# Performance work log

Hardware: AMD Instinct MI355X
Metric: run time of the kernel (lower is better)

## Reference

```python
import jax, jax.numpy as jnp
import numpy as np

B, C, H, W = 32, 256, 7, 7
HEADS = 8
DIM_HEAD = 64
INNER = HEADS * DIM_HEAD  # 512
N_ANGLES = 16
KS = 5
GROUPS = 32
EPS = 1e-5


def setup_inputs() -> dict:
    key = jax.random.key(0)
    ks = jax.random.split(key, 16)
    w = lambda k, shp: jax.random.normal(k, shp, jnp.float32) * 0.05
    return {
        'x': jax.random.normal(ks[0], (B, C, H, W), jnp.float32),
        'gn_g': jnp.ones((C,), jnp.float32), 'gn_b': jnp.zeros((C,), jnp.float32),
        'sa_w1': w(ks[1], (C // 8, C)), 'sa_b1': jnp.zeros((C // 8,), jnp.float32),
        'sa_w2': w(ks[2], (C, C // 8)), 'sa_b2': jnp.zeros((C,), jnp.float32),
        'sa_gn_g': jnp.ones((C,), jnp.float32), 'sa_gn_b': jnp.zeros((C,), jnp.float32),
        'ra_gn_g': jnp.ones((C,), jnp.float32), 'ra_gn_b': jnp.zeros((C,), jnp.float32),
        'ra_qkv_w': w(ks[3], (3 * C, C)),
        'ra_proj_w': w(ks[4], (C, C)), 'ra_proj_b': jnp.zeros((C,), jnp.float32),
        'aa_ln_g': jnp.ones((C,), jnp.float32), 'aa_ln_b': jnp.zeros((C,), jnp.float32),
        'aa_qkv_w': w(ks[5], (3 * INNER, C)),
        'aa_relpos': w(ks[6], (2 * 7 - 1, 2 * 7 - 1, HEADS)),
        'aa_out_w': w(ks[7], (C, INNER)), 'aa_out_b': jnp.zeros((C,), jnp.float32),
        'ad_dir_w': w(ks[8], (N_ANGLES, C, C, KS, KS)),
        'ad_ap_w1': w(ks[9], (128, C)), 'ad_ap_b1': jnp.zeros((128,), jnp.float32),
        'ad_ap_w2': w(ks[10], (N_ANGLES, 128)), 'ad_ap_b2': jnp.zeros((N_ANGLES,), jnp.float32),
        'ad_proj_w': w(ks[11], (C, C)), 'ad_proj_b': jnp.zeros((C,), jnp.float32),
        'gate_w': w(ks[12], (4, C)), 'gate_b': jnp.zeros((4,), jnp.float32),
        'proj_w': w(ks[13], (C, C)), 'proj_b': jnp.zeros((C,), jnp.float32),
    }


def _gn(x, g, b):
    Bx, Cx, Hx, Wx = x.shape
    xr = x.reshape(Bx, GROUPS, -1)
    m = xr.mean(-1, keepdims=True)
    v = xr.var(-1, keepdims=True)
    xn = ((xr - m) * jax.lax.rsqrt(v + EPS)).reshape(Bx, Cx, Hx, Wx)
    return xn * g[None, :, None, None] + b[None, :, None, None]


def _c1(x, w, b=None):
    y = jnp.einsum('bchw,oc->bohw', x, w)
    return y if b is None else y + b[None, :, None, None]


def _rot_attn_pass(x, qkv_w):
    Bx, Cx, Hx, Wx = x.shape
    d = Cx // HEADS
    q, k, v = jnp.split(_c1(x, qkv_w), 3, axis=1)
    sh = lambda t: t.reshape(Bx, HEADS, d, Hx * Wx).transpose(0, 1, 3, 2)  # b h n d
    q, k, v = sh(q), sh(k), sh(v)
    a = jax.nn.softmax(jnp.einsum('bhid,bhjd->bhij', q, k) * (d ** -0.5), axis=-1)
    o = jnp.einsum('bhij,bhjd->bhid', a, v)
    return o.transpose(0, 1, 3, 2).reshape(Bx, Cx, Hx, Wx)


def _forward(x, gn_g, gn_b, sa_w1, sa_b1, sa_w2, sa_b2, sa_gn_g, sa_gn_b,
             ra_gn_g, ra_gn_b, ra_qkv_w, ra_proj_w, ra_proj_b,
             aa_ln_g, aa_ln_b, aa_qkv_w, aa_relpos, aa_out_w, aa_out_b,
             ad_dir_w, ad_ap_w1, ad_ap_b1, ad_ap_w2, ad_ap_b2, ad_proj_w, ad_proj_b,
             gate_w, gate_b, proj_w, proj_b):
    normed = _gn(x, gn_g, gn_b)

    # --- SpatialAttention branch ---
    wts = jax.nn.sigmoid(_c1(jax.nn.relu(_c1(normed, sa_w1, sa_b1)), sa_w2, sa_b2))
    spatial = _gn(normed * wts + normed, sa_gn_g, sa_gn_b)

    # --- RotationAwareAttention branch: 4 rot90 passes, max-fused ---
    xr = _gn(normed, ra_gn_g, ra_gn_b)
    r0 = _rot_attn_pass(xr, ra_qkv_w)
    r1 = jnp.rot90(_rot_attn_pass(jnp.rot90(xr, 1, (2, 3)), ra_qkv_w), 3, (2, 3))
    r2 = jnp.rot90(_rot_attn_pass(jnp.rot90(xr, 2, (2, 3)), ra_qkv_w), 2, (2, 3))
    r3 = jnp.rot90(_rot_attn_pass(jnp.rot90(xr, 3, (2, 3)), ra_qkv_w), 1, (2, 3))
    mx = jnp.maximum(jnp.maximum(r0, r1), jnp.maximum(r2, r3))
    rotation = _c1(mx, ra_proj_w, ra_proj_b) + normed

    # --- AngleAwareSelfAttention branch (rel-pos-biased MHSA over 49 tokens) ---
    Nn = H * W
    t = normed.reshape(B, C, Nn).transpose(0, 2, 1)  # [B,N,C]
    mu = t.mean(-1, keepdims=True)
    var = t.var(-1, keepdims=True)
    tn = (t - mu) * jax.lax.rsqrt(var + EPS) * aa_ln_g + aa_ln_b
    q, k, v = jnp.split(jnp.einsum('bnc,oc->bno', tn, aa_qkv_w), 3, axis=-1)
    sh = lambda u: u.reshape(B, Nn, HEADS, DIM_HEAD).transpose(0, 2, 1, 3)
    q, k, v = sh(q), sh(k), sh(v)
    dots = jnp.einsum('bhid,bhjd->bhij', q, k) * (DIM_HEAD ** -0.5)
    idx = jnp.arange(Nn)
    yi, xi = idx // W, idx % W
    dy = yi[None, :] - yi[:, None] + (H - 1)  # offsets into 13x13 table
    dx = xi[None, :] - xi[:, None] + (W - 1)
    bias = aa_relpos[dy, dx].transpose(2, 0, 1)[None]  # [1,heads,N,N]
    attn = jax.nn.softmax(dots + bias, axis=-1)
    o = jnp.einsum('bhij,bhjd->bhid', attn, v).transpose(0, 2, 1, 3).reshape(B, Nn, INNER)
    o = jnp.einsum('bni,oi->bno', o, aa_out_w) + aa_out_b
    angle = o.transpose(0, 2, 1).reshape(B, C, H, W) + normed

    # --- AngleAdaptiveAttention branch: 16 directional 5x5 convs + learned softmax gate ---
    dir_out = jax.lax.conv_general_dilated(
        normed, ad_dir_w.reshape(N_ANGLES * C, C, KS, KS), (1, 1), 'SAME',
        dimension_numbers=('NCHW', 'OIHW', 'NCHW')).reshape(B, N_ANGLES, C, H, W)
    gap = normed.mean((2, 3))  # [B,C]
    h1 = jax.nn.relu(gap @ ad_ap_w1.T + ad_ap_b1)
    aw = jax.nn.softmax(h1 @ ad_ap_w2.T + ad_ap_b2, axis=1)  # [B,16]
    comb = jnp.einsum('bkchw,bk->bchw', dir_out, aw)
    adaptive = _c1(comb, ad_proj_w, ad_proj_b) + normed

    # --- gated fusion ---
    gates = jax.nn.softmax(_c1(x, gate_w, gate_b), axis=1)  # [B,4,H,W]
    fused = (spatial * gates[:, 0:1] + rotation * gates[:, 1:2]
             + angle * gates[:, 2:3] + adaptive * gates[:, 3:4])
    return _c1(fused, proj_w, proj_b) + x


def reference(x, gn_g, gn_b, sa_w1, sa_b1, sa_w2, sa_b2, sa_gn_g, sa_gn_b,
              ra_gn_g, ra_gn_b, ra_qkv_w, ra_proj_w, ra_proj_b,
              aa_ln_g, aa_ln_b, aa_qkv_w, aa_relpos, aa_out_w, aa_out_b,
              ad_dir_w, ad_ap_w1, ad_ap_b1, ad_ap_w2, ad_ap_b2, ad_proj_w, ad_proj_b,
              gate_w, gate_b, proj_w, proj_b):
    return _forward(x, gn_g, gn_b, sa_w1, sa_b1, sa_w2, sa_b2, sa_gn_g, sa_gn_b,
                    ra_gn_g, ra_gn_b, ra_qkv_w, ra_proj_w, ra_proj_b,
                    aa_ln_g, aa_ln_b, aa_qkv_w, aa_relpos, aa_out_w, aa_out_b,
                    ad_dir_w, ad_ap_w1, ad_ap_b1, ad_ap_w2, ad_ap_b2, ad_proj_w, ad_proj_b,
                    gate_w, gate_b, proj_w, proj_b)
```

## Files before the change

kernel.cpp:

```cpp
#include <hip/hip_runtime.h>

#define EPS 1e-5f
typedef unsigned short u16;
typedef unsigned int u32;
typedef float f32x4 __attribute__((ext_vector_type(4)));
typedef short bf16x8 __attribute__((ext_vector_type(8)));
typedef unsigned int u32x2 __attribute__((ext_vector_type(2)));

__device__ __forceinline__ float bf2f(u16 h){
  return __uint_as_float(((u32)h) << 16);
}
__device__ __forceinline__ u16 f2bf(float f){
  u32 u = __float_as_uint(f);
  u += 0x7fffu + ((u >> 16) & 1u);
  return (u16)(u >> 16);
}
__device__ __forceinline__ u32 pk2(float lo, float hi){
  return ((u32)f2bf(hi) << 16) | (u32)f2bf(lo);
}
union BF8 { bf16x8 v; u32 u[4]; };

__global__ __launch_bounds__(256) void k_prep1(
    const float* __restrict__ x, const float* __restrict__ gn_g, const float* __restrict__ gn_b,
    const float* __restrict__ ra_g, const float* __restrict__ ra_b,
    float* __restrict__ normed, float* __restrict__ xr, float* __restrict__ gap)
{
  int ch = blockIdx.x, b = blockIdx.y;
  int c0 = ch * 32;
  __shared__ float xs[1568], ns[1568];
  const float* xb = x + ((size_t)b * 256 + c0) * 49;
  for (int i = threadIdx.x; i < 1568; i += 256) xs[i] = xb[i];
  __syncthreads();
  int wv = threadIdx.x >> 6, lane = threadIdx.x & 63;
  const float* gsrc = xs + wv * 392;
  float* ndst = ns + wv * 392;
  float s = 0.f, ss = 0.f;
  for (int i = lane; i < 392; i += 64){ float v = gsrc[i]; s += v; ss += v * v; }
  for (int off = 32; off; off >>= 1){ s += __shfl_down(s, off); ss += __shfl_down(ss, off); }
  s = __shfl(s, 0); ss = __shfl(ss, 0);
  float m = s / 392.f, rs = rsqrtf(ss / 392.f - m * m + EPS);
  for (int i = lane; i < 392; i += 64){
    int c = c0 + wv * 8 + i / 49;
    ndst[i] = (gsrc[i] - m) * rs * gn_g[c] + gn_b[c];
  }
  __syncthreads();
  float* nb = normed + ((size_t)b * 256 + c0) * 49;
  for (int i = threadIdx.x; i < 1568; i += 256) nb[i] = ns[i];
  if (threadIdx.x < 32){
    float g2 = 0.f; const float* rp = ns + threadIdx.x * 49;
    for (int p = 0; p < 49; p++) g2 += rp[p];
    gap[(size_t)b * 256 + c0 + threadIdx.x] = g2 * (1.f / 49.f);
  }
  s = 0.f; ss = 0.f;
  for (int i = lane; i < 392; i += 64){ float v = ndst[i]; s += v; ss += v * v; }
  for (int off = 32; off; off >>= 1){ s += __shfl_down(s, off); ss += __shfl_down(ss, off); }
  s = __shfl(s, 0); ss = __shfl(ss, 0);
  m = s / 392.f; rs = rsqrtf(ss / 392.f - m * m + EPS);
  float* xrb = xr + ((size_t)b * 256 + c0) * 49;
  for (int i = lane; i < 392; i += 64){
    int c = c0 + wv * 8 + i / 49;
    xrb[wv * 392 + i] = (ndst[i] - m) * rs * ra_g[c] + ra_b[c];
  }
}

__device__ void dev_pos(
    const float* __restrict__ x, const float* __restrict__ normed,
    const float* __restrict__ gate_w, const float* __restrict__ gate_b,
    float* __restrict__ gates_g, float* __restrict__ lnm_g, float* __restrict__ lnr_g,
    int pc, int b, float* sm)
{
  float* gw = sm;
  for (int i = threadIdx.x; i < 1024; i += 256) gw[i] = gate_w[i];
  __syncthreads();
  int wv = threadIdx.x >> 6, lane = threadIdx.x & 63;
  for (int pi = wv; pi < 7; pi += 4){
    int p = pc * 7 + pi;
    const float* nb = normed + (size_t)b * 12544 + p;
    const float* xb = x + (size_t)b * 12544 + p;
    float s = 0.f, ss = 0.f, g0 = 0.f, g1 = 0.f, g2 = 0.f, g3 = 0.f;
    for (int c = lane; c < 256; c += 64){
      float nv = nb[c * 49];
      float xv = xb[c * 49];
      s += nv; ss += nv * nv;
      g0 += xv * gw[c]; g1 += xv * gw[256 + c];
      g2 += xv * gw[512 + c]; g3 += xv * gw[768 + c];
    }
    for (int off = 32; off; off >>= 1){
      s += __shfl_down(s, off); ss += __shfl_down(ss, off);
      g0 += __shfl_down(g0, off); g1 += __shfl_down(g1, off);
      g2 += __shfl_down(g2, off); g3 += __shfl_down(g3, off);
    }
    if (lane == 0){
      float mu = s / 256.f;
      lnm_g[b * 49 + p] = mu;
      lnr_g[b * 49 + p] = rsqrtf(ss / 256.f - mu * mu + EPS);
      g0 += gate_b[0]; g1 += gate_b[1]; g2 += gate_b[2]; g3 += gate_b[3];
      float mx = fmaxf(fmaxf(g0, g1), fmaxf(g2, g3));
      float e0 = __expf(g0 - mx), e1 = __expf(g1 - mx), e2 = __expf(g2 - mx), e3 = __expf(g3 - mx);
      float inv = 1.f / (e0 + e1 + e2 + e3);
      float* gg = gates_g + (size_t)b * 196 + p;
      gg[0] = e0 * inv; gg[49] = e1 * inv; gg[98] = e2 * inv; gg[147] = e3 * inv;
    }
  }
}

__device__ void dev_h1aw(
    const float* __restrict__ normed, const float* __restrict__ sa_w1, const float* __restrict__ sa_b1,
    const float* __restrict__ ap_w1, const float* __restrict__ ap_b1,
    const float* __restrict__ ap_w2, const float* __restrict__ ap_b2,
    const float* __restrict__ gap_g,
    float* __restrict__ h1_g, float* __restrict__ aw_g,
    int xb2, int b, float* sm)
{
  int t = threadIdx.x;
  if (xb2 == 7){
    float* gaps = sm; float* h = sm + 256; float* lg = sm + 384;
    gaps[t] = gap_g[b * 256 + t];
    __syncthreads();
    if (t < 128){
      float s = ap_b1[t];
      const float* wr = ap_w1 + t * 256;
      #pragma unroll 4
      for (int c = 0; c < 256; c++) s += gaps[c] * wr[c];
      h[t] = fmaxf(s, 0.f);
    }
    __syncthreads();
    if (t < 16){
      float s = ap_b2[t];
      const float* wr = ap_w2 + t * 128;
      #pragma unroll 4
      for (int o = 0; o < 128; o++) s += h[o] * wr[o];
      lg[t] = s;
    }
    __syncthreads();
    if (t == 0){
      float mx = -1e30f;
      for (int k = 0; k < 16; k++) mx = fmaxf(mx, lg[k]);
      float e[16], smm = 0.f;
      for (int k = 0; k < 16; k++){ e[k] = __expf(lg[k] - mx); smm += e[k]; }
      float inv = 1.f / smm;
      for (int k = 0; k < 16; k++) aw_g[b * 16 + k] = e[k] * inv;
    }
    return;
  }
  float* w1t = sm;
  float* ns2 = sm + 8448;
  int p0 = xb2 * 7;
  for (int i = t; i < 8192; i += 256){
    int o = i >> 8, c = i & 255;
    w1t[c * 33 + o] = sa_w1[i];
  }
  for (int i = t; i < 1792; i += 256){
    int c = i / 7, pl = i - c * 7;
    ns2[i] = normed[(size_t)b * 12544 + c * 49 + p0 + pl];
  }
  __syncthreads();
  if (t < 224){
    int pl = t >> 5, o = t & 31;
    float s = sa_b1[o];
    #pragma unroll 8
    for (int c = 0; c < 256; c++) s += ns2[c * 7 + pl] * w1t[c * 33 + o];
    h1_g[(size_t)b * 1568 + (p0 + pl) * 32 + o] = fmaxf(s, 0.f);
  }
}

__global__ __launch_bounds__(256) void k_pre2(
    const float* __restrict__ x, const float* __restrict__ normed,
    const float* __restrict__ gate_w, const float* __restrict__ gate_b,
    const float* __restrict__ sa_w1, const float* __restrict__ sa_b1,
    const float* __restrict__ ap_w1, const float* __restrict__ ap_b1,
    const float* __restrict__ ap_w2, const float* __restrict__ ap_b2,
    const float* __restrict__ gap_g,
    float* __restrict__ gates_g, float* __restrict__ lnm_g, float* __restrict__ lnr_g,
    float* __restrict__ h1_g, float* __restrict__ aw_g)
{
  __shared__ float sm[10240];
  int bx = blockIdx.x, b = blockIdx.y;
  if (bx < 7)
    dev_pos(x, normed, gate_w, gate_b, gates_g, lnm_g, lnr_g, bx, b, sm);
  else
    dev_h1aw(normed, sa_w1, sa_b1, ap_w1, ap_b1, ap_w2, ap_b2, gap_g, h1_g, aw_g, bx - 7, b, sm);
}

__device__ void dev_spatial(
    const float* __restrict__ normed, const float* __restrict__ h1_g,
    const float* __restrict__ sa_w2, const float* __restrict__ sa_b2,
    const float* __restrict__ sa_g, const float* __restrict__ sa_bb,
    float* __restrict__ spat_g, int gc, int b, float* sm)
{
  float* h1s = sm;
  float* w2s = sm + 1617;
  int t = threadIdx.x;
  for (int i = t; i < 1568; i += 256){
    int p = i >> 5, o = i & 31;
    h1s[p * 33 + o] = h1_g[(size_t)b * 1568 + i];
  }
  for (int i = t; i < 1024; i += 256) w2s[i] = sa_w2[gc * 1024 + i];
  __syncthreads();
  int wv = t >> 6, lane = t & 63;
  int cg0 = wv * 8;
  const float* nb = normed + (size_t)b * 12544 + (gc * 32 + cg0) * 49;
  float tmp[7];
  float s = 0.f, ss = 0.f;
  #pragma unroll
  for (int j = 0; j < 7; j++){
    int i = lane + 64 * j;
    float v = 0.f;
    if (i < 392){
      int c = i / 49;
      const float* wr = w2s + (cg0 + c) * 32;
      const float* hp = h1s + (i - c * 49) * 33;
      float d = sa_b2[gc * 32 + cg0 + c];
      #pragma unroll
      for (int o = 0; o < 32; o++) d += hp[o] * wr[o];
      v = nb[i] * (1.f + 1.f / (1.f + __expf(-d)));
      s += v; ss += v * v;
    }
    tmp[j] = v;
  }
  for (int off = 32; off; off >>= 1){ s += __shfl_down(s, off); ss += __shfl_down(ss, off); }
  s = __shfl(s, 0); ss = __shfl(ss, 0);
  float m = s / 392.f, rs = rsqrtf(ss / 392.f - m * m + EPS);
  float* sb = spat_g + (size_t)b * 12544 + (gc * 32 + cg0) * 49;
  #pragma unroll
  for (int j = 0; j < 7; j++){
    int i = lane + 64 * j;
    if (i < 392){
      int c = gc * 32 + cg0 + i / 49;
      sb[i] = (tmp[j] - m) * rs * sa_g[c] + sa_bb[c];
    }
  }
}

__device__ void dev_weff(
    const float* __restrict__ W, const float* __restrict__ aw, u16* __restrict__ weff, int bx)
{
  const size_t t = ((size_t)bx * 256 + threadIdx.x) * 4;
  float4 A[16];
  #pragma unroll
  for (int k = 0; k < 16; k++) A[k] = *(const float4*)(W + (size_t)k * 1638400 + t);
  #pragma unroll 1
  for (int b = 0; b < 32; b++){
    float s0 = 0.f, s1 = 0.f, s2 = 0.f, s3 = 0.f;
    #pragma unroll
    for (int k = 0; k < 16; k++){
      float a = aw[b * 16 + k];
      s0 += a * A[k].x; s1 += a * A[k].y; s2 += a * A[k].z; s3 += a * A[k].w;
    }
    u32x2 o; o.x = pk2(s0, s1); o.y = pk2(s2, s3);
    __builtin_nontemporal_store(o, (u32x2*)(weff + (size_t)b * 1638400 + t));
  }
}

__device__ void dev_im2col(
    const float* __restrict__ normed, u16* __restrict__ xim, int p, int b, float* sm)
{
  u16* row = (u16*)sm;
  int ci = threadIdx.x;
  int py = p / 7, px = p - py * 7;
  const float* nb = normed + (size_t)b * 12544 + ci * 49;
  u16* rp = row + ci * 25;
  #pragma unroll
  for (int sy = 0; sy < 5; sy++){
    int iy = py + sy - 2;
    #pragma unroll
    for (int sx = 0; sx < 5; sx++){
      int ix = px + sx - 2;
      float v = (iy >= 0 && iy < 7 && ix >= 0 && ix < 7) ? nb[iy * 7 + ix] : 0.f;
      rp[sy * 5 + sx] = f2bf(v);
    }
  }
  __syncthreads();
  const u32* rs = (const u32*)row;
  u32* od = (u32*)(xim + (size_t)(b * 49 + p) * 6400);
  for (int i = threadIdx.x; i < 3200; i += 256) od[i] = rs[i];
}

__device__ __forceinline__ void mfma_gemm_dev(
    const float* __restrict__ W, const float* __restrict__ bias,
    const float* __restrict__ act, const float* __restrict__ res,
    float* __restrict__ out, int M, int K, int m0blk, int p0, int b,
    const float* __restrict__ lnm, const float* __restrict__ lnr,
    const float* __restrict__ lng, const float* __restrict__ lnb)
{
  int wv = threadIdx.x >> 6, lane = threadIdx.x & 63;
  int lo = lane & 15, hi = lane >> 4;
  int m0 = m0blk + wv * 32;
  int p = p0 + lo;
  bool pok = p < 49;
  const float* ab = act + (size_t)b * K * 49;
  float lm = 0.f, lr = 0.f;
  if (lng && pok){ lm = lnm[p]; lr = lnr[p]; }
  f32x4 acc0 = {0.f, 0.f, 0.f, 0.f};
  f32x4 acc1 = {0.f, 0.f, 0.f, 0.f};
  const float* wr0 = W + (size_t)(m0 + lo) * K + hi * 8;
  const float* wr1 = W + (size_t)(m0 + 16 + lo) * K + hi * 8;
  for (int k0 = 0; k0 < K; k0 += 32){
    int kb = k0 + hi * 8;
    float4 a0lo = *(const float4*)(wr0 + k0);
    float4 a0hi = *(const float4*)(wr0 + k0 + 4);
    float4 a1lo = *(const float4*)(wr1 + k0);
    float4 a1hi = *(const float4*)(wr1 + k0 + 4);
    float bv[8];
    if (pok){
      const float* ap = ab + (size_t)kb * 49 + p;
      #pragma unroll
      for (int i = 0; i < 8; i++) bv[i] = ap[i * 49];
      if (lng){
        #pragma unroll
        for (int i = 0; i < 8; i++) bv[i] = (bv[i] - lm) * lr * lng[kb + i] + lnb[kb + i];
      }
    } else {
      #pragma unroll
      for (int i = 0; i < 8; i++) bv[i] = 0.f;
    }
    BF8 A0, A1, B;
    A0.u[0] = pk2(a0lo.x, a0lo.y); A0.u[1] = pk2(a0lo.z, a0lo.w);
    A0.u[2] = pk2(a0hi.x, a0hi.y); A0.u[3] = pk2(a0hi.z, a0hi.w);
    A1.u[0] = pk2(a1lo.x, a1lo.y); A1.u[1] = pk2(a1lo.z, a1lo.w);
    A1.u[2] = pk2(a1hi.x, a1hi.y); A1.u[3] = pk2(a1hi.z, a1hi.w);
    B.u[0] = pk2(bv[0], bv[1]); B.u[1] = pk2(bv[2], bv[3]);
    B.u[2] = pk2(bv[4], bv[5]); B.u[3] = pk2(bv[6], bv[7]);
    acc0 = __builtin_amdgcn_mfma_f32_16x16x32_bf16(A0.v, B.v, acc0, 0, 0, 0);
    acc1 = __builtin_amdgcn_mfma_f32_16x16x32_bf16(A1.v, B.v, acc1, 0, 0, 0);
  }
  if (pok){
    #pragma unroll
    for (int r = 0; r < 4; r++){
      int m = m0 + hi * 4 + r;
      size_t idx = ((size_t)b * M + m) * 49 + p;
      float v = acc0[r] + (bias ? bias[m] : 0.f);
      if (res) v += res[idx];
      out[idx] = v;
      int m2 = m + 16;
      size_t idx2 = idx + 16 * 49;
      float v2 = acc1[r] + (bias ? bias[m2] : 0.f);
      if (res) v2 += res[idx2];
      out[idx2] = v2;
    }
  }
}

__global__ __launch_bounds__(256) void k_mega1(
    const float* __restrict__ ad_dir_w, const float* __restrict__ aw, u16* __restrict__ weff,
    const float* __restrict__ ra_w, const float* __restrict__ aa_w,
    const float* __restrict__ xr, const float* __restrict__ normed,
    const float* __restrict__ lnm, const float* __restrict__ lnr,
    const float* __restrict__ ln_g, const float* __restrict__ ln_b,
    float* __restrict__ ra_qkv, float* __restrict__ aa_qkv,
    u16* __restrict__ xim,
    const float* __restrict__ h1_g, const float* __restrict__ sa_w2, const float* __restrict__ sa_b2,
    const float* __restrict__ sa_g, const float* __restrict__ sa_bb, float* __restrict__ spat_g)
{
  __shared__ float sm[3300];
  int id = blockIdx.x;
  if (id < 1600){
    dev_weff(ad_dir_w, aw, weff, id);
  } else if (id < 3904){
    int q = id - 1600;
    int bx = q % 72, b = q / 72;
    if (bx < 24){
      int m0 = (bx >> 2) * 128, p0 = (bx & 3) * 16;
      mfma_gemm_dev(ra_w, nullptr, xr, nullptr, ra_qkv, 768, 256, m0, p0, b,
                    nullptr, nullptr, nullptr, nullptr);
    } else {
      int bx2 = bx - 24;
      int m0 = (bx2 >> 2) * 128, p0 = (bx2 & 3) * 16;
      mfma_gemm_dev(aa_w, nullptr, normed, nullptr, aa_qkv, 1536, 256, m0, p0, b,
                    lnm + b * 49, lnr + b * 49, ln_g, ln_b);
    }
  } else if (id < 5472){
    int q = id - 3904;
    dev_im2col(normed, xim, q % 49, q / 49, sm);
  } else {
    int q = id - 5472;
    dev_spatial(normed, h1_g, sa_w2, sa_b2, sa_g, sa_bb, spat_g, q % 8, q / 8, sm);
  }
}

__device__ void dev_conv(
    const u16* __restrict__ weff, const u16* __restrict__ xim, float* __restrict__ partial,
    int bx, int b)
{
  int mblk = bx >> 3, kp = bx & 7;
  int wv = threadIdx.x >> 6, lane = threadIdx.x & 63;
  int lo = lane & 15, hi = lane >> 4;
  int co0 = mblk * 128 + wv * 32;
  const u16* wr0 = weff + (size_t)b * 1638400 + (size_t)(co0 + lo) * 6400 + kp * 800 + hi * 8;
  const u16* wr1 = wr0 + 16 * 6400;
  const u16* xb = xim + (size_t)b * 313600 + (size_t)lo * 6400 + kp * 800 + hi * 8;
  f32x4 acc[2][4];
  #pragma unroll
  for (int mi = 0; mi < 2; mi++)
    #pragma unroll
    for (int pi = 0; pi < 4; pi++) acc[mi][pi] = (f32x4){0.f, 0.f, 0.f, 0.f};
  #pragma unroll 1
  for (int ks = 0; ks < 25; ks++){
    int k0 = ks * 32;
    bf16x8 A0 = __builtin_nontemporal_load((const bf16x8*)(wr0 + k0));
    bf16x8 A1 = __builtin_nontemporal_load((const bf16x8*)(wr1 + k0));
    bf16x8 B0 = *(const bf16x8*)(xb + k0);
    bf16x8 B1 = *(const bf16x8*)(xb + 16 * 6400 + k0);
    bf16x8 B2 = *(const bf16x8*)(xb + 32 * 6400 + k0);
    bf16x8 B3 = *(const bf16x8*)(xb + 48 * 6400 + k0);
    acc[0][0] = __builtin_amdgcn_mfma_f32_16x16x32_bf16(A0, B0, acc[0][0], 0, 0, 0);
    acc[0][1] = __builtin_amdgcn_mfma_f32_16x16x32_bf16(A0, B1, acc[0][1], 0, 0, 0);
    acc[0][2] = __builtin_amdgcn_mfma_f32_16x16x32_bf16(A0, B2, acc[0][2], 0, 0, 0);
    acc[0][3] = __builtin_amdgcn_mfma_f32_16x16x32_bf16(A0, B3, acc[0][3], 0, 0, 0);
    acc[1][0] = __builtin_amdgcn_mfma_f32_16x16x32_bf16(A1, B0, acc[1][0], 0, 0, 0);
    acc[1][1] = __builtin_amdgcn_mfma_f32_16x16x32_bf16(A1, B1, acc[1][1], 0, 0, 0);
    acc[1][2] = __builtin_amdgcn_mfma_f32_16x16x32_bf16(A1, B2, acc[1][2], 0, 0, 0);
    acc[1][3] = __builtin_amdgcn_mfma_f32_16x16x32_bf16(A1, B3, acc[1][3], 0, 0, 0);
  }
  float* pb = partial + ((size_t)kp * 32 + b) * 12544;
  #pragma unroll
  for (int mi = 0; mi < 2; mi++){
    #pragma unroll
    for (int pi = 0; pi < 4; pi++){
      int p = pi * 16 + lo;
      if (p < 49){
        #pragma unroll
        for (int r = 0; r < 4; r++){
          int co = co0 + mi * 16 + hi * 4 + r;
          pb[co * 49 + p] = acc[mi][pi][r];
        }
      }
    }
  }
}

__device__ __forceinline__ void softmax_rows(float* sc, int tid)
{
  int r = tid >> 2, q = tid & 3;
  if (r < 49){
    float* row = sc + r * 52;
    float mx = -1e30f;
    for (int j = q; j < 49; j += 4) mx = fmaxf(mx, row[j]);
    mx = fmaxf(mx, __shfl_xor(mx, 1));
    mx = fmaxf(mx, __shfl_xor(mx, 2));
    float sm = 0.f;
    for (int j = q; j < 49; j += 4){ float e = __expf(row[j] - mx); row[j] = e; sm += e; }
    sm += __shfl_xor(sm, 1);
    sm += __shfl_xor(sm, 2);
    float inv = 1.f / sm;
    for (int j = q; j < 49; j += 4) row[j] *= inv;
  }
}

__device__ void dev_attn(
    const float* __restrict__ ra_qkv, const float* __restrict__ aa_qkv,
    const float* __restrict__ relpos,
    float* __restrict__ r0, float* __restrict__ ao,
    int xb2, int b, float* sm)
{
  if (xb2 < 8){
    int hd = xb2;
    float* qs = sm; float* ks = sm + 1617; float* vs = sm + 3234; float* sc = sm + 4851;
    const float* base = ra_qkv + (size_t)b * 768 * 49;
    for (int i = threadIdx.x; i < 1568; i += 256){
      int d = i / 49, tok = i - d * 49;
      qs[tok * 33 + d] = base[(hd * 32 + d) * 49 + tok];
      ks[tok * 33 + d] = base[(256 + hd * 32 + d) * 49 + tok];
      vs[tok * 33 + d] = base[(512 + hd * 32 + d) * 49 + tok];
    }
    __syncthreads();
    const float scale = 0.17677669529663687f;
    for (int it = threadIdx.x; it < 2401; it += 256){
      int i = it / 49, j = it - i * 49;
      float s = 0.f;
      #pragma unroll
      for (int d = 0; d < 32; d++) s += qs[i * 33 + d] * ks[j * 33 + d];
      sc[i * 52 + j] = s * scale;
    }
    __syncthreads();
    softmax_rows(sc, threadIdx.x);
    __syncthreads();
    for (int it = threadIdx.x; it < 1568; it += 256){
      int d = it / 49, i = it - d * 49;
      float o = 0.f;
      for (int j = 0; j < 49; j++) o += sc[i * 52 + j] * vs[j * 33 + d];
      r0[((size_t)b * 256 + hd * 32 + d) * 49 + i] = o;
    }
  } else {
    int hd = xb2 - 8;
    float* qs = sm; float* ks = sm + 3185; float* vs = sm + 6370; float* sc = sm + 9555;
    const float* base = aa_qkv + (size_t)b * 1536 * 49;
    for (int i = threadIdx.x; i < 3136; i += 256){
      int d = i / 49, tok = i - d * 49;
      qs[tok * 65 + d] = base[(hd * 64 + d) * 49 + tok];
      ks[tok * 65 + d] = base[(512 + hd * 64 + d) * 49 + tok];
      vs[tok * 65 + d] = base[(1024 + hd * 64 + d) * 49 + tok];
    }
    __syncthreads();
    for (int it = threadIdx.x; it < 2401; it += 256){
      int i = it / 49, j = it - i * 49;
      float s = 0.f;
      #pragma unroll
      for (int d = 0; d < 64; d++) s += qs[i * 65 + d] * ks[j * 65 + d];
      int dy = j / 7 - i / 7 + 6, dx = j % 7 - i % 7 + 6;
      sc[i * 52 + j] = s * 0.125f + relpos[(dy * 13 + dx) * 8 + hd];
    }
    __syncthreads();
    softmax_rows(sc, threadIdx.x);
    __syncthreads();
    for (int it = threadIdx.x; it < 3136; it += 256){
      int d = it / 49, i = it - d * 49;
      float o = 0.f;
      for (int j = 0; j < 49; j++) o += sc[i * 52 + j] * vs[j * 65 + d];
      ao[((size_t)b * 512 + hd * 64 + d) * 49 + i] = o;
    }
  }
}

__global__ __launch_bounds__(256) void k_mega2(
    const u16* __restrict__ weff, const u16* __restrict__ xim, float* __restrict__ partial,
    const float* __restrict__ ra_qkv, const float* __restrict__ aa_qkv,
    const float* __restrict__ relpos, float* __restrict__ r0, float* __restrict__ ao)
{
  __shared__ float sm[12103];
  int id = blockIdx.x;
  if (id < 512){
    dev_conv(weff, xim, partial, id % 16, id / 16);
  } else {
    int q = id - 512;
    dev_attn(ra_qkv, aa_qkv, relpos, r0, ao, q % 16, q / 16, sm);
  }
}

__global__ __launch_bounds__(256) void k_conv_reduce(
    const float* __restrict__ part, float* __restrict__ comb)
{
  int i = blockIdx.x * 256 + threadIdx.x;
  if (i >= 100352) return;
  float a0 = 0.f, a1 = 0.f, a2 = 0.f, a3 = 0.f;
  #pragma unroll
  for (int p = 0; p < 8; p++){
    float4 v = ((const float4*)part)[(size_t)p * 100352 + i];
    a0 += v.x; a1 += v.y; a2 += v.z; a3 += v.w;
  }
  float4 o; o.x = a0; o.y = a1; o.z = a2; o.w = a3;
  ((float4*)comb)[i] = o;
}

__global__ __launch_bounds__(256) void k_proj3(
    const float* __restrict__ ra_pw, const float* __restrict__ ra_pb, const float* __restrict__ r0,
    const float* __restrict__ aa_ow, const float* __restrict__ aa_ob, const float* __restrict__ aa_o,
    const float* __restrict__ ad_pw, const float* __restrict__ ad_pb, const float* __restrict__ comb,
    const float* __restrict__ normed,
    float* __restrict__ rotf, float* __restrict__ angf, float* __restrict__ adpf)
{
  int bx = blockIdx.x, b = blockIdx.y;
  if (bx < 8){
    int m0 = (bx >> 2) * 128, p0 = (bx & 3) * 16;
    mfma_gemm_dev(ra_pw, ra_pb, r0, normed, rotf, 256, 256, m0, p0, b,
                  nullptr, nullptr, nullptr, nullptr);
  } else if (bx < 16){
    int bx2 = bx - 8;
    int m0 = (bx2 >> 2) * 128, p0 = (bx2 & 3) * 16;
    mfma_gemm_dev(aa_ow, aa_ob, aa_o, normed, angf, 256, 512, m0, p0, b,
                  nullptr, nullptr, nullptr, nullptr);
  } else {
    int bx2 = bx - 16;
    int m0 = (bx2 >> 2) * 128, p0 = (bx2 & 3) * 16;
    mfma_gemm_dev(ad_pw, ad_pb, comb, normed, adpf, 256, 256, m0, p0, b,
                  nullptr, nullptr, nullptr, nullptr);
  }
}

__global__ __launch_bounds__(256) void k_final(
    const float* __restrict__ proj_w, const float* __restrict__ proj_b,
    const float* __restrict__ spat, const float* __restrict__ rotf,
    const float* __restrict__ angf, const float* __restrict__ adpf,
    const float* __restrict__ gates, const float* __restrict__ x,
    float* __restrict__ out)
{
  int bx = blockIdx.x, b = blockIdx.y;
  int wv = threadIdx.x >> 6, lane = threadIdx.x & 63;
  int lo = lane & 15, hi = lane >> 4;
  int m0 = (bx >> 2) * 128 + wv * 32;
  int p0 = (bx & 3) * 16;
  int p = p0 + lo;
  bool pok = p < 49;
  float g0 = 0.f, g1 = 0.f, g2 = 0.f, g3 = 0.f;
  if (pok){
    const float* g = gates + (size_t)b * 196 + p;
    g0 = g[0]; g1 = g[49]; g2 = g[98]; g3 = g[147];
  }
  size_t boff = (size_t)b * 12544;
  f32x4 acc0 = {0.f, 0.f, 0.f, 0.f};
  f32x4 acc1 = {0.f, 0.f, 0.f, 0.f};
  const float* wr0 = proj_w + (size_t)(m0 + lo) * 256 + hi * 8;
  const float* wr1 = wr0 + 16 * 256;
  for (int k0 = 0; k0 < 256; k0 += 32){
    int kb = k0 + hi * 8;
    float4 a0lo = *(const float4*)(wr0 + k0);
    float4 a0hi = *(const float4*)(wr0 + k0 + 4);
    float4 a1lo = *(const float4*)(wr1 + k0);
    float4 a1hi = *(const float4*)(wr1 + k0 + 4);
    float bv[8];
    if (pok){
      size_t base = boff + (size_t)kb * 49 + p;
      #pragma unroll
      for (int i = 0; i < 8; i++){
        size_t idx = base + (size_t)i * 49;
        bv[i] = spat[idx] * g0 + rotf[idx] * g1 + angf[idx] * g2 + adpf[idx] * g3;
      }
    } else {
      #pragma unroll
      for (int i = 0; i < 8; i++) bv[i] = 0.f;
    }
    BF8 A0, A1, B;
    A0.u[0] = pk2(a0lo.x, a0lo.y); A0.u[1] = pk2(a0lo.z, a0lo.w);
    A0.u[2] = pk2(a0hi.x, a0hi.y); A0.u[3] = pk2(a0hi.z, a0hi.w);
    A1.u[0] = pk2(a1lo.x, a1lo.y); A1.u[1] = pk2(a1lo.z, a1lo.w);
    A1.u[2] = pk2(a1hi.x, a1hi.y); A1.u[3] = pk2(a1hi.z, a1hi.w);
    B.u[0] = pk2(bv[0], bv[1]); B.u[1] = pk2(bv[2], bv[3]);
    B.u[2] = pk2(bv[4], bv[5]); B.u[3] = pk2(bv[6], bv[7]);
    acc0 = __builtin_amdgcn_mfma_f32_16x16x32_bf16(A0.v, B.v, acc0, 0, 0, 0);
    acc1 = __builtin_amdgcn_mfma_f32_16x16x32_bf16(A1.v, B.v, acc1, 0, 0, 0);
  }
  if (pok){
    #pragma unroll
    for (int r = 0; r < 4; r++){
      int m = m0 + hi * 4 + r;
      size_t idx = boff + (size_t)m * 49 + p;
      out[idx] = acc0[r] + proj_b[m] + x[idx];
      int m2 = m + 16;
      size_t idx2 = idx + 16 * 49;
      out[idx2] = acc1[r] + proj_b[m2] + x[idx2];
    }
  }
}

extern "C" void kernel_launch(void* const* d_in, const int* in_sizes, int n_in,
                              void* d_out, int out_size, void* d_ws, size_t ws_size,
                              hipStream_t stream)
{
  const float* x        = (const float*)d_in[0];
  const float* gn_g     = (const float*)d_in[1];
  const float* gn_b     = (const float*)d_in[2];
  const float* sa_w1    = (const float*)d_in[3];
  const float* sa_b1    = (const float*)d_in[4];
  const float* sa_w2    = (const float*)d_in[5];
  const float* sa_b2    = (const float*)d_in[6];
  const float* sa_gn_g  = (const float*)d_in[7];
  const float* sa_gn_b  = (const float*)d_in[8];
  const float* ra_gn_g  = (const float*)d_in[9];
  const float* ra_gn_b  = (const float*)d_in[10];
  const float* ra_qkv_w = (const float*)d_in[11];
  const float* ra_proj_w= (const float*)d_in[12];
  const float* ra_proj_b= (const float*)d_in[13];
  const float* aa_ln_g  = (const float*)d_in[14];
  const float* aa_ln_b  = (const float*)d_in[15];
  const float* aa_qkv_w = (const float*)d_in[16];
  const float* aa_relpos= (const float*)d_in[17];
  const float* aa_out_w = (const float*)d_in[18];
  const float* aa_out_b = (const float*)d_in[19];
  const float* ad_dir_w = (const float*)d_in[20];
  const float* ad_ap_w1 = (const float*)d_in[21];
  const float* ad_ap_b1 = (const float*)d_in[22];
  const float* ad_ap_w2 = (const float*)d_in[23];
  const float* ad_ap_b2 = (const float*)d_in[24];
  const float* ad_proj_w= (const float*)d_in[25];
  const float* ad_proj_b= (const float*)d_in[26];
  const float* gate_w   = (const float*)d_in[27];
  const float* gate_b   = (const float*)d_in[28];
  const float* proj_w   = (const float*)d_in[29];
  const float* proj_b   = (const float*)d_in[30];

  char* ws = (char*)d_ws;
  float* normed    = (float*)(ws + 0);
  float* xr        = (float*)(ws + 1605632);
  float* h1_g      = (float*)(ws + 3211264);
  float* lnm       = (float*)(ws + 3420160);
  float* lnr       = (float*)(ws + 3426560);
  float* spatial   = (float*)(ws + 4816896);
  float* rotf      = (float*)(ws + 6422528);
  float* anglef    = (float*)(ws + 8028160);
  float* adaptf    = (float*)(ws + 9633792);
  float* r0        = (float*)(ws + 12845056);
  float* gap       = (float*)(ws + 14450688);
  float* aw        = (float*)(ws + 14483456);
  float* gates     = (float*)(ws + 14485504);
  float* ra_qkv    = (float*)(ws + 14510592);
  float* aa_qkv    = (float*)(ws + 19327488);
  float* aa_o      = (float*)(ws + 28961280);
  float* comb      = (float*)(ws + 32172544);
  float* partial   = (float*)(ws + 33778176);
  u16*   xim       = (u16*)  (ws + 46623232);
  u16*   weff      = (u16*)  (ws + 66693632);

  float* out = (float*)d_out;

  k_prep1<<<dim3(8, 32), 256, 0, stream>>>(x, gn_g, gn_b, ra_gn_g, ra_gn_b, normed, xr, gap);
  k_pre2<<<dim3(15, 32), 256, 0, stream>>>(x, normed, gate_w, gate_b,
                                           sa_w1, sa_b1, ad_ap_w1, ad_ap_b1, ad_ap_w2, ad_ap_b2,
                                           gap, gates, lnm, lnr, h1_g, aw);
  k_mega1<<<dim3(5728), 256, 0, stream>>>(ad_dir_w, aw, weff,
                                          ra_qkv_w, aa_qkv_w, xr, normed,
                                          lnm, lnr, aa_ln_g, aa_ln_b, ra_qkv, aa_qkv,
                                          xim,
                                          h1_g, sa_w2, sa_b2, sa_gn_g, sa_gn_b, spatial);
  k_mega2<<<dim3(1024), 256, 0, stream>>>(weff, xim, partial,
                                          ra_qkv, aa_qkv, aa_relpos, r0, aa_o);
  k_conv_reduce<<<dim3(392), 256, 0, stream>>>(partial, comb);
  k_proj3<<<dim3(24, 32), 256, 0, stream>>>(ra_proj_w, ra_proj_b, r0,
                                            aa_out_w, aa_out_b, aa_o,
                                            ad_proj_w, ad_proj_b, comb,
                                            normed, rotf, anglef, adaptf);
  k_final<<<dim3(8, 32), 256, 0, stream>>>(proj_w, proj_b, spatial, rotf, anglef, adaptf,
                                           gates, x, out);
}
```

Measured before the change: 265.7 us.

## Fuse conv split-K reduction into projection GEMM and rebalance mega-kernel block mix

Removes the separate split-K reduction kernel. The adaptive projection GEMM now sums the eight conv partials directly while it loads its B operand, which saves one launch and one write/read of the combined buffer. The spatial-branch blocks move from the first mega-kernel into the second. Both mega-kernels also permute block IDs with a modular multiplier so the different task types interleave across the grid instead of running in contiguous phases. In exchange, each projection block that handles the adaptive branch reads the partials eight times over with strided loads, and the permutation must be a bijection to stay correct.

```diff
diff --git a/kernel.cpp b/kernel.cpp
--- a/kernel.cpp
+++ b/kernel.cpp
@@ -281,7 +281,8 @@
     const float* __restrict__ act, const float* __restrict__ res,
     float* __restrict__ out, int M, int K, int m0blk, int p0, int b,
     const float* __restrict__ lnm, const float* __restrict__ lnr,
-    const float* __restrict__ lng, const float* __restrict__ lnb)
+    const float* __restrict__ lng, const float* __restrict__ lnb,
+    const float* __restrict__ part8 = nullptr)
 {
   int wv = threadIdx.x >> 6, lane = threadIdx.x & 63;
   int lo = lane & 15, hi = lane >> 4;
@@ -303,12 +304,23 @@
     float4 a1hi = *(const float4*)(wr1 + k0 + 4);
     float bv[8];
     if (pok){
-      const float* ap = ab + (size_t)kb * 49 + p;
-      #pragma unroll
-      for (int i = 0; i < 8; i++) bv[i] = ap[i * 49];
-      if (lng){
+      if (part8){
+        const float* pp = part8 + (size_t)b * 12544 + (size_t)kb * 49 + p;
         #pragma unroll
-        for (int i = 0; i < 8; i++) bv[i] = (bv[i] - lm) * lr * lng[kb + i] + lnb[kb + i];
+        for (int i = 0; i < 8; i++){
+          float s = 0.f;
+          #pragma unroll
+          for (int kp = 0; kp < 8; kp++) s += pp[(size_t)kp * 401408 + i * 49];
+          bv[i] = s;
+        }
+      } else {
+        const float* ap = ab + (size_t)kb * 49 + p;
+        #pragma unroll
+        for (int i = 0; i < 8; i++) bv[i] = ap[i * 49];
+        if (lng){
+          #pragma unroll
+          for (int i = 0; i < 8; i++) bv[i] = (bv[i] - lm) * lr * lng[kb + i] + lnb[kb + i];
+        }
       }
     } else {
       #pragma unroll
@@ -338,43 +350,6 @@
       if (res) v2 += res[idx2];
       out[idx2] = v2;
     }
-  }
-}
-
-__global__ __launch_bounds__(256) void k_mega1(
-    const float* __restrict__ ad_dir_w, const float* __restrict__ aw, u16* __restrict__ weff,
-    const float* __restrict__ ra_w, const float* __restrict__ aa_w,
-    const float* __restrict__ xr, const float* __restrict__ normed,
-    const float* __restrict__ lnm, const float* __restrict__ lnr,
-    const float* __restrict__ ln_g, const float* __restrict__ ln_b,
-    float* __restrict__ ra_qkv, float* __restrict__ aa_qkv,
-    u16* __restrict__ xim,
-    const float* __restrict__ h1_g, const float* __restrict__ sa_w2, const float* __restrict__ sa_b2,
-    const float* __restrict__ sa_g, const float* __restrict__ sa_bb, float* __restrict__ spat_g)
-{
-  __shared__ float sm[3300];
-  int id = blockIdx.x;
-  if (id < 1600){
-    dev_weff(ad_dir_w, aw, weff, id);
-  } else if (id < 3904){
-    int q = id - 1600;
-    int bx = q % 72, b = q / 72;
-    if (bx < 24){
-      int m0 = (bx >> 2) * 128, p0 = (bx & 3) * 16;
-      mfma_gemm_dev(ra_w, nullptr, xr, nullptr, ra_qkv, 768, 256, m0, p0, b,
-                    nullptr, nullptr, nullptr, nullptr);
-    } else {
-      int bx2 = bx - 24;
-      int m0 = (bx2 >> 2) * 128, p0 = (bx2 & 3) * 16;
-      mfma_gemm_dev(aa_w, nullptr, normed, nullptr, aa_qkv, 1536, 256, m0, p0, b,
-                    lnm + b * 49, lnr + b * 49, ln_g, ln_b);
-    }
-  } else if (id < 5472){
-    int q = id - 3904;
-    dev_im2col(normed, xim, q % 49, q / 49, sm);
-  } else {
-    int q = id - 5472;
-    dev_spatial(normed, h1_g, sa_w2, sa_b2, sa_g, sa_bb, spat_g, q % 8, q / 8, sm);
   }
 }
 
@@ -512,40 +487,64 @@
   }
 }
 
+__global__ __launch_bounds__(256) void k_mega1(
+    const float* __restrict__ ad_dir_w, const float* __restrict__ aw, u16* __restrict__ weff,
+    const float* __restrict__ ra_w, const float* __restrict__ aa_w,
+    const float* __restrict__ xr, const float* __restrict__ normed,
+    const float* __restrict__ lnm, const float* __restrict__ lnr,
+    const float* __restrict__ ln_g, const float* __restrict__ ln_b,
+    float* __restrict__ ra_qkv, float* __restrict__ aa_qkv,
+    u16* __restrict__ xim)
+{
+  __shared__ float sm[3300];
+  int id = (int)(((long long)blockIdx.x * 2003) % 5472);
+  if (id < 1600){
+    dev_weff(ad_dir_w, aw, weff, id);
+  } else if (id < 3904){
+    int q = id - 1600;
+    int bx = q % 72, b = q / 72;
+    if (bx < 24){
+      int m0 = (bx >> 2) * 128, p0 = (bx & 3) * 16;
+      mfma_gemm_dev(ra_w, nullptr, xr, nullptr, ra_qkv, 768, 256, m0, p0, b,
+                    nullptr, nullptr, nullptr, nullptr);
+    } else {
+      int bx2 = bx - 24;
+      int m0 = (bx2 >> 2) * 128, p0 = (bx2 & 3) * 16;
+      mfma_gemm_dev(aa_w, nullptr, normed, nullptr, aa_qkv, 1536, 256, m0, p0, b,
+                    lnm + b * 49, lnr + b * 49, ln_g, ln_b);
+    }
+  } else {
+    int q = id - 3904;
+    dev_im2col(normed, xim, q % 49, q / 49, sm);
+  }
+}
+
 __global__ __launch_bounds__(256) void k_mega2(
     const u16* __restrict__ weff, const u16* __restrict__ xim, float* __restrict__ partial,
     const float* __restrict__ ra_qkv, const float* __restrict__ aa_qkv,
-    const float* __restrict__ relpos, float* __restrict__ r0, float* __restrict__ ao)
+    const float* __restrict__ relpos, float* __restrict__ r0, float* __restrict__ ao,
+    const float* __restrict__ normed, const float* __restrict__ h1_g,
+    const float* __restrict__ sa_w2, const float* __restrict__ sa_b2,
+    const float* __restrict__ sa_g, const float* __restrict__ sa_bb,
+    float* __restrict__ spat_g)
 {
   __shared__ float sm[12103];
-  int id = blockIdx.x;
+  int id = (int)(((long long)blockIdx.x * 521) % 1280);
   if (id < 512){
     dev_conv(weff, xim, partial, id % 16, id / 16);
-  } else {
+  } else if (id < 1024){
     int q = id - 512;
     dev_attn(ra_qkv, aa_qkv, relpos, r0, ao, q % 16, q / 16, sm);
-  }
-}
-
-__global__ __launch_bounds__(256) void k_conv_reduce(
-    const float* __restrict__ part, float* __restrict__ comb)
-{
-  int i = blockIdx.x * 256 + threadIdx.x;
-  if (i >= 100352) return;
-  float a0 = 0.f, a1 = 0.f, a2 = 0.f, a3 = 0.f;
-  #pragma unroll
-  for (int p = 0; p < 8; p++){
-    float4 v = ((const float4*)part)[(size_t)p * 100352 + i];
-    a0 += v.x; a1 += v.y; a2 += v.z; a3 += v.w;
-  }
-  float4 o; o.x = a0; o.y = a1; o.z = a2; o.w = a3;
-  ((float4*)comb)[i] = o;
+  } else {
+    int q = id - 1024;
+    dev_spatial(normed, h1_g, sa_w2, sa_b2, sa_g, sa_bb, spat_g, q % 8, q / 8, sm);
+  }
 }
 
 __global__ __launch_bounds__(256) void k_proj3(
     const float* __restrict__ ra_pw, const float* __restrict__ ra_pb, const float* __restrict__ r0,
     const float* __restrict__ aa_ow, const float* __restrict__ aa_ob, const float* __restrict__ aa_o,
-    const float* __restrict__ ad_pw, const float* __restrict__ ad_pb, const float* __restrict__ comb,
+    const float* __restrict__ ad_pw, const float* __restrict__ ad_pb, const float* __restrict__ partial,
     const float* __restrict__ normed,
     float* __restrict__ rotf, float* __restrict__ angf, float* __restrict__ adpf)
 {
@@ -562,8 +561,8 @@
   } else {
     int bx2 = bx - 16;
     int m0 = (bx2 >> 2) * 128, p0 = (bx2 & 3) * 16;
-    mfma_gemm_dev(ad_pw, ad_pb, comb, normed, adpf, 256, 256, m0, p0, b,
-                  nullptr, nullptr, nullptr, nullptr);
+    mfma_gemm_dev(ad_pw, ad_pb, partial , normed, adpf, 256, 256, m0, p0, b,
+                  nullptr, nullptr, nullptr, nullptr, partial);
   }
 }
 
@@ -685,7 +684,6 @@
   float* ra_qkv    = (float*)(ws + 14510592);
   float* aa_qkv    = (float*)(ws + 19327488);
   float* aa_o      = (float*)(ws + 28961280);
-  float* comb      = (float*)(ws + 32172544);
   float* partial   = (float*)(ws + 33778176);
   u16*   xim       = (u16*)  (ws + 46623232);
   u16*   weff      = (u16*)  (ws + 66693632);
@@ -696,17 +694,16 @@
   k_pre2<<<dim3(15, 32), 256, 0, stream>>>(x, normed, gate_w, gate_b,
                                            sa_w1, sa_b1, ad_ap_w1, ad_ap_b1, ad_ap_w2, ad_ap_b2,
                                            gap, gates, lnm, lnr, h1_g, aw);
-  k_mega1<<<dim3(5728), 256, 0, stream>>>(ad_dir_w, aw, weff,
+  k_mega1<<<dim3(5472), 256, 0, stream>>>(ad_dir_w, aw, weff,
                                           ra_qkv_w, aa_qkv_w, xr, normed,
                                           lnm, lnr, aa_ln_g, aa_ln_b, ra_qkv, aa_qkv,
-                                          xim,
-                                          h1_g, sa_w2, sa_b2, sa_gn_g, sa_gn_b, spatial);
-  k_mega2<<<dim3(1024), 256, 0, stream>>>(weff, xim, partial,
-                                          ra_qkv, aa_qkv, aa_relpos, r0, aa_o);
-  k_conv_reduce<<<dim3(392), 256, 0, stream>>>(partial, comb);
+                                          xim);
+  k_mega2<<<dim3(1280), 256, 0, stream>>>(weff, xim, partial,
+                                          ra_qkv, aa_qkv, aa_relpos, r0, aa_o,
+                                          normed, h1_g, sa_w2, sa_b2, sa_gn_g, sa_gn_b, spatial);
   k_proj3<<<dim3(24, 32), 256, 0, stream>>>(ra_proj_w, ra_proj_b, r0,
                                             aa_out_w, aa_out_b, aa_o,
-                                            ad_proj_w, ad_proj_b, comb,
+                                            ad_proj_w, ad_proj_b, partial,
                                             normed, rotf, anglef, adaptf);
   k_final<<<dim3(8, 32), 256, 0, stream>>>(proj_w, proj_b, spatial, rotf, anglef, adaptf,
                                            gates, x, out);
```

Measured after the change: 250.5 us. 1.06x faster.
